# Performance work log

Measured on AMD Instinct MI355X. Metric: run time of the kernel, lower is better.

The kernel has to match this reference:

```python
import jax, jax.numpy as jnp
import numpy as np

EPS = 1e-8


def setup_inputs() -> dict:
    key = jax.random.key(0)
    k1, k2, k3, k4 = jax.random.split(key, 4)
    B, N, M, C = 512, 512, 128, 1024
    addr = M + 6  # read head: k(M) + beta(1) + g(1) + s(3) + gamma(1)
    controller_out = jax.random.normal(k1, (B, C), dtype=jnp.float32)
    prev_w = jax.random.uniform(k2, (B, N), dtype=jnp.float32)
    prev_w = prev_w / prev_w.sum(axis=1, keepdims=True)  # valid weighting
    memory_state = jax.random.normal(k3, (B, N, M), dtype=jnp.float32)
    W_fc = jax.random.normal(k4, (C, addr), dtype=jnp.float32) * 0.02
    b_fc = jnp.zeros((addr,), dtype=jnp.float32)
    return {"controller_out": controller_out, "prev_w": prev_w,
            "memory_state": memory_state, "W_fc": W_fc, "b_fc": b_fc}


def reference(controller_out, prev_w, memory_state, W_fc, b_fc):
    M = memory_state.shape[2]
    out = controller_out @ W_fc + b_fc  # [B, M+6]
    k = out[:, :M]                                   # key
    beta = jax.nn.softplus(out[:, M:M + 1])          # key strength
    g = jax.nn.sigmoid(out[:, M + 1:M + 2])          # interpolation gate
    s = jax.nn.softmax(out[:, M + 2:M + 5], axis=1)  # 3-tap shift weights
    gamma = 1.0 + jax.nn.softplus(out[:, M + 5:M + 6])

    # Content addressing (Eq. 5-6): cosine similarity + sharpened softmax
    norm_k = jnp.linalg.norm(k, axis=1, keepdims=True) + EPS      # [B,1]
    norm_mem = jnp.linalg.norm(memory_state, axis=2) + EPS        # [B,N]
    sim = jnp.einsum('bnm,bm->bn', memory_state, k) / (norm_k * norm_mem)
    w_c = jax.nn.softmax(beta * sim, axis=1)

    # Interpolation (Eq. 7)
    w_g = g * w_c + (1.0 - g) * prev_w

    # Circular 3-tap shift (Eq. 8): vectorized roll instead of per-slot loop
    w_s = (s[:, 0:1] * jnp.roll(w_g, 1, axis=1)
           + s[:, 1:2] * w_g
           + s[:, 2:3] * jnp.roll(w_g, -1, axis=1))

    # Sharpening (Eq. 9)
    w_pow = w_s ** gamma
    w = w_pow / (w_pow.sum(axis=1, keepdims=True) + EPS)

    # Read vector (read head)
    read_vec = jnp.einsum('bn,bnm->bm', w, memory_state)
    return (read_vec, w)
```

## Files before the change

### kernel.cpp

```cpp
#include <hip/hip_runtime.h>
#include <math.h>

#define BB   512
#define NN   512
#define MM   128
#define CC   1024
#define ADDR 134
#define EPSF 1e-8f
#define NT   1024

__device__ __forceinline__ float softplus_f(float x) {
    return fmaxf(x, 0.0f) + log1pf(expf(-fabsf(x)));
}

__global__ __launch_bounds__(NT) void ntm_head_kernel(
    const float* __restrict__ co,
    const float* __restrict__ prev_w,
    const float* __restrict__ mem,
    const float* __restrict__ W_fc,
    const float* __restrict__ b_fc,
    float* __restrict__ out_rv,
    float* __restrict__ out_w)
{
    __shared__ __align__(16) float s_co[CC];
    __shared__ __align__(16) float s_k[MM];
    __shared__ float s_extra[8];
    __shared__ float s_fcpart[4 * ADDR];
    __shared__ float s_bsim[NN];
    __shared__ float s_wg[NN];
    __shared__ float s_w[NN];
    __shared__ __align__(16) float s_part[32 * MM];
    __shared__ float s_red[16];
    __shared__ float s_params[8];

    const int t = threadIdx.x;
    const int b = blockIdx.x;
    const int wv = t >> 6;

    s_co[t] = co[(size_t)b * CC + t];
    __syncthreads();

    {
        const int q = t >> 8;
        const int j = t & 255;
        if (j < ADDR) {
            float a0 = 0.f, a1 = 0.f, a2 = 0.f, a3 = 0.f;
            const float* Wp = W_fc + j;
            const int c0 = q * 256;
            for (int c = c0; c < c0 + 256; c += 4) {
                float4 cv = *(const float4*)(s_co + c);
                a0 = fmaf(cv.x, Wp[(size_t)(c + 0) * ADDR], a0);
                a1 = fmaf(cv.y, Wp[(size_t)(c + 1) * ADDR], a1);
                a2 = fmaf(cv.z, Wp[(size_t)(c + 2) * ADDR], a2);
                a3 = fmaf(cv.w, Wp[(size_t)(c + 3) * ADDR], a3);
            }
            s_fcpart[q * ADDR + j] = (a0 + a1) + (a2 + a3);
        }
    }
    __syncthreads();
    if (t < ADDR) {
        float r = s_fcpart[t] + s_fcpart[ADDR + t] + s_fcpart[2 * ADDR + t]
                + s_fcpart[3 * ADDR + t] + b_fc[t];
        if (t < MM) s_k[t] = r; else s_extra[t - MM] = r;
    }
    __syncthreads();

    {
        float v = (t < MM) ? s_k[t] * s_k[t] : 0.0f;
        #pragma unroll
        for (int off = 32; off >= 1; off >>= 1) v += __shfl_xor(v, off, 64);
        if ((t & 63) == 0) s_red[wv] = v;
        __syncthreads();
        if (t == 0) {
            float ks = 0.f;
            #pragma unroll
            for (int i = 0; i < 16; ++i) ks += s_red[i];
            float norm_k = sqrtf(ks) + EPSF;
            float beta = softplus_f(s_extra[0]);
            float g = 1.0f / (1.0f + expf(-s_extra[1]));
            float e0 = s_extra[2], e1 = s_extra[3], e2 = s_extra[4];
            float mx = fmaxf(e0, fmaxf(e1, e2));
            float x0 = expf(e0 - mx), x1 = expf(e1 - mx), x2 = expf(e2 - mx);
            float inv = 1.0f / (x0 + x1 + x2);
            s_params[0] = beta / norm_k;
            s_params[1] = g;
            s_params[2] = x0 * inv;
            s_params[3] = x1 * inv;
            s_params[4] = x2 * inv;
            s_params[5] = 1.0f + softplus_f(s_extra[5]);
        }
    }
    __syncthreads();

    const float bnk = s_params[0];
    const float4* memb = (const float4*)(mem + (size_t)b * NN * MM);

    {
        const int gi = t >> 5;
        const int l  = t & 31;
        float4 kv = ((const float4*)s_k)[l];
        for (int n0 = gi; n0 < NN; n0 += 128) {
            float4 a0 = memb[(size_t)(n0      ) * 32 + l];
            float4 a1 = memb[(size_t)(n0 + 32 ) * 32 + l];
            float4 a2 = memb[(size_t)(n0 + 64 ) * 32 + l];
            float4 a3 = memb[(size_t)(n0 + 96 ) * 32 + l];
            float d0 = a0.x*kv.x + a0.y*kv.y + a0.z*kv.z + a0.w*kv.w;
            float q0 = a0.x*a0.x + a0.y*a0.y + a0.z*a0.z + a0.w*a0.w;
            float d1 = a1.x*kv.x + a1.y*kv.y + a1.z*kv.z + a1.w*kv.w;
            float q1 = a1.x*a1.x + a1.y*a1.y + a1.z*a1.z + a1.w*a1.w;
            float d2 = a2.x*kv.x + a2.y*kv.y + a2.z*kv.z + a2.w*kv.w;
            float q2 = a2.x*a2.x + a2.y*a2.y + a2.z*a2.z + a2.w*a2.w;
            float d3 = a3.x*kv.x + a3.y*kv.y + a3.z*kv.z + a3.w*kv.w;
            float q3 = a3.x*a3.x + a3.y*a3.y + a3.z*a3.z + a3.w*a3.w;
            #pragma unroll
            for (int off = 16; off >= 1; off >>= 1) {
                d0 += __shfl_xor(d0, off, 64); q0 += __shfl_xor(q0, off, 64);
                d1 += __shfl_xor(d1, off, 64); q1 += __shfl_xor(q1, off, 64);
                d2 += __shfl_xor(d2, off, 64); q2 += __shfl_xor(q2, off, 64);
                d3 += __shfl_xor(d3, off, 64); q3 += __shfl_xor(q3, off, 64);
            }
            if (l == 0) {
                s_bsim[n0      ] = bnk * d0 / (sqrtf(q0) + EPSF);
                s_bsim[n0 + 32 ] = bnk * d1 / (sqrtf(q1) + EPSF);
                s_bsim[n0 + 64 ] = bnk * d2 / (sqrtf(q2) + EPSF);
                s_bsim[n0 + 96 ] = bnk * d3 / (sqrtf(q3) + EPSF);
            }
        }
    }
    __syncthreads();

    {
        const bool act = (t < NN);
        float bv = act ? s_bsim[t] : -INFINITY;
        float pw = act ? prev_w[(size_t)b * NN + t] : 0.0f;

        float m = bv;
        #pragma unroll
        for (int off = 32; off >= 1; off >>= 1) m = fmaxf(m, __shfl_xor(m, off, 64));
        if ((t & 63) == 0) s_red[wv] = m;
        __syncthreads();
        float M8 = -INFINITY;
        #pragma unroll
        for (int i = 0; i < 8; ++i) M8 = fmaxf(M8, s_red[i]);
        __syncthreads();

        float e = act ? expf(bv - M8) : 0.0f;
        float ls = e;
        #pragma unroll
        for (int off = 32; off >= 1; off >>= 1) ls += __shfl_xor(ls, off, 64);
        if ((t & 63) == 0) s_red[wv] = ls;
        __syncthreads();
        float S = 0.f;
        #pragma unroll
        for (int i = 0; i < 16; ++i) S += s_red[i];
        __syncthreads();

        const float invS = 1.0f / S;
        const float g = s_params[1];
        float wg = fmaf(g, e * invS, (1.0f - g) * pw);
        if (act) s_wg[t] = wg;
        __syncthreads();

        const float sh0 = s_params[2], sh1 = s_params[3], sh2 = s_params[4];
        const float gamma = s_params[5];
        float wp = 0.0f;
        if (act) {
            float ws = sh0 * s_wg[(t + NN - 1) & (NN - 1)] + sh1 * wg
                     + sh2 * s_wg[(t + 1) & (NN - 1)];
            wp = powf(ws, gamma);
        }
        float lz = wp;
        #pragma unroll
        for (int off = 32; off >= 1; off >>= 1) lz += __shfl_xor(lz, off, 64);
        if ((t & 63) == 0) s_red[wv] = lz;
        __syncthreads();
        float Z = 0.f;
        #pragma unroll
        for (int i = 0; i < 16; ++i) Z += s_red[i];

        const float invZ = 1.0f / (Z + EPSF);
        if (act) {
            float w = wp * invZ;
            s_w[t] = w;
            out_w[(size_t)b * NN + t] = w;
        }
    }
    __syncthreads();

    {
        const int q = t >> 5;
        const int l = t & 31;
        float4 acc = make_float4(0.f, 0.f, 0.f, 0.f);
        const int nb = q * 16;
        #pragma unroll
        for (int i = 0; i < 16; i += 4) {
            const int n = nb + i;
            float4 a0 = memb[(size_t)(n    ) * 32 + l];
            float4 a1 = memb[(size_t)(n + 1) * 32 + l];
            float4 a2 = memb[(size_t)(n + 2) * 32 + l];
            float4 a3 = memb[(size_t)(n + 3) * 32 + l];
            float w0 = s_w[n], w1 = s_w[n + 1], w2 = s_w[n + 2], w3 = s_w[n + 3];
            acc.x = fmaf(w0, a0.x, acc.x); acc.y = fmaf(w0, a0.y, acc.y);
            acc.z = fmaf(w0, a0.z, acc.z); acc.w = fmaf(w0, a0.w, acc.w);
            acc.x = fmaf(w1, a1.x, acc.x); acc.y = fmaf(w1, a1.y, acc.y);
            acc.z = fmaf(w1, a1.z, acc.z); acc.w = fmaf(w1, a1.w, acc.w);
            acc.x = fmaf(w2, a2.x, acc.x); acc.y = fmaf(w2, a2.y, acc.y);
            acc.z = fmaf(w2, a2.z, acc.z); acc.w = fmaf(w2, a2.w, acc.w);
            acc.x = fmaf(w3, a3.x, acc.x); acc.y = fmaf(w3, a3.y, acc.y);
            acc.z = fmaf(w3, a3.z, acc.z); acc.w = fmaf(w3, a3.w, acc.w);
        }
        *((float4*)&s_part[q * MM + l * 4]) = acc;
        __syncthreads();
        if (t < MM) {
            float r = 0.f;
            #pragma unroll
            for (int q2 = 0; q2 < 32; ++q2) r += s_part[q2 * MM + t];
            out_rv[(size_t)b * MM + t] = r;
        }
    }
}

extern "C" void kernel_launch(void* const* d_in, const int* in_sizes, int n_in,
                              void* d_out, int out_size, void* d_ws, size_t ws_size,
                              hipStream_t stream) {
    const float* co     = (const float*)d_in[0];
    const float* prev_w = (const float*)d_in[1];
    const float* mem    = (const float*)d_in[2];
    const float* W_fc   = (const float*)d_in[3];
    const float* b_fc   = (const float*)d_in[4];
    float* out = (float*)d_out;
    ntm_head_kernel<<<BB, NT, 0, stream>>>(co, prev_w, mem, W_fc, b_fc,
                                           out, out + (size_t)BB * MM);
}
```

Baseline: 245.9 us.

## Split FC projection into separate kernel and restructure similarity pass with 4-lane rows

Moves the controller FC projection and head-parameter computation into a separate kernel that handles two batch rows per block and writes key and parameters to a workspace. The main kernel then reads those from the workspace instead of recomputing the FC, which frees the 1024-thread blocks from the serial FC phase. The similarity pass changes to four lanes per memory row with the row-max reduction fused in, removing a sync and one reduction pass. This adds a second launch and a workspace round trip, and the FC kernel has low parallelism with only 192 threads per block.

```diff
diff --git a/kernel.cpp b/kernel.cpp
--- a/kernel.cpp
+++ b/kernel.cpp
@@ -7,88 +7,111 @@
 #define CC   1024
 #define ADDR 134
 #define EPSF 1e-8f
-#define NT   1024
+#define WSSTRIDE 136
 
 __device__ __forceinline__ float softplus_f(float x) {
     return fmaxf(x, 0.0f) + log1pf(expf(-fabsf(x)));
 }
 
-__global__ __launch_bounds__(NT) void ntm_head_kernel(
+__global__ __launch_bounds__(192) void ntm_fc_kernel(
     const float* __restrict__ co,
+    const float* __restrict__ W_fc,
+    const float* __restrict__ b_fc,
+    float* __restrict__ ws)
+{
+    __shared__ __align__(16) float s_co[2 * CC];
+    __shared__ float s_nr[2][2];
+    __shared__ float s_ex[2][8];
+
+    const int t = threadIdx.x;
+    const int b0 = blockIdx.x * 2;
+
+    {
+        const float4* src = (const float4*)(co + (size_t)b0 * CC);
+        float4* dst = (float4*)s_co;
+        for (int i = t; i < 512; i += 192) dst[i] = src[i];
+    }
+    __syncthreads();
+
+    float k0 = 0.f, k1 = 0.f;
+    if (t < ADDR) {
+        float a00 = 0.f, a01 = 0.f, a10 = 0.f, a11 = 0.f;
+        const float* Wj = W_fc + t;
+        for (int c = 0; c < CC; c += 8) {
+            float wv[8];
+            #pragma unroll
+            for (int i = 0; i < 8; ++i) wv[i] = Wj[(size_t)(c + i) * ADDR];
+            #pragma unroll
+            for (int i = 0; i < 8; ++i) {
+                if (i & 1) { a01 = fmaf(wv[i], s_co[c + i], a01);
+                             a11 = fmaf(wv[i], s_co[CC + c + i], a11); }
+                else       { a00 = fmaf(wv[i], s_co[c + i], a00);
+                             a10 = fmaf(wv[i], s_co[CC + c + i], a10); }
+            }
+        }
+        float bias = b_fc[t];
+        k0 = a00 + a01 + bias;
+        k1 = a10 + a11 + bias;
+        if (t >= MM) { s_ex[0][t - MM] = k0; s_ex[1][t - MM] = k1; }
+        else {
+            ws[(size_t)b0 * WSSTRIDE + t] = k0;
+            ws[(size_t)(b0 + 1) * WSSTRIDE + t] = k1;
+        }
+    }
+    if (t < MM) {
+        float v0 = k0 * k0, v1 = k1 * k1;
+        #pragma unroll
+        for (int off = 32; off >= 1; off >>= 1) {
+            v0 += __shfl_xor(v0, off, 64);
+            v1 += __shfl_xor(v1, off, 64);
+        }
+        if ((t & 63) == 0) { s_nr[t >> 6][0] = v0; s_nr[t >> 6][1] = v1; }
+    }
+    __syncthreads();
+    if (t < 2) {
+        float ks = s_nr[0][t] + s_nr[1][t];
+        float norm_k = sqrtf(ks) + EPSF;
+        float beta = softplus_f(s_ex[t][0]);
+        float g = 1.0f / (1.0f + expf(-s_ex[t][1]));
+        float e0 = s_ex[t][2], e1 = s_ex[t][3], e2 = s_ex[t][4];
+        float mx = fmaxf(e0, fmaxf(e1, e2));
+        float x0 = expf(e0 - mx), x1 = expf(e1 - mx), x2 = expf(e2 - mx);
+        float inv = 1.0f / (x0 + x1 + x2);
+        float* p = ws + (size_t)(b0 + t) * WSSTRIDE + MM;
+        p[0] = beta / norm_k;
+        p[1] = g;
+        p[2] = x0 * inv;
+        p[3] = x1 * inv;
+        p[4] = x2 * inv;
+        p[5] = 1.0f + softplus_f(s_ex[t][5]);
+    }
+}
+
+__global__ __launch_bounds__(1024) void ntm_main_kernel(
     const float* __restrict__ prev_w,
     const float* __restrict__ mem,
-    const float* __restrict__ W_fc,
-    const float* __restrict__ b_fc,
+    const float* __restrict__ ws,
     float* __restrict__ out_rv,
     float* __restrict__ out_w)
 {
-    __shared__ __align__(16) float s_co[CC];
     __shared__ __align__(16) float s_k[MM];
-    __shared__ float s_extra[8];
-    __shared__ float s_fcpart[4 * ADDR];
+    __shared__ float s_params[8];
     __shared__ float s_bsim[NN];
     __shared__ float s_wg[NN];
     __shared__ float s_w[NN];
     __shared__ __align__(16) float s_part[32 * MM];
-    __shared__ float s_red[16];
-    __shared__ float s_params[8];
+    __shared__ float s_redA[16];
+    __shared__ float s_redB[16];
 
     const int t = threadIdx.x;
     const int b = blockIdx.x;
     const int wv = t >> 6;
 
-    s_co[t] = co[(size_t)b * CC + t];
-    __syncthreads();
-
-    {
-        const int q = t >> 8;
-        const int j = t & 255;
-        if (j < ADDR) {
-            float a0 = 0.f, a1 = 0.f, a2 = 0.f, a3 = 0.f;
-            const float* Wp = W_fc + j;
-            const int c0 = q * 256;
-            for (int c = c0; c < c0 + 256; c += 4) {
-                float4 cv = *(const float4*)(s_co + c);
-                a0 = fmaf(cv.x, Wp[(size_t)(c + 0) * ADDR], a0);
-                a1 = fmaf(cv.y, Wp[(size_t)(c + 1) * ADDR], a1);
-                a2 = fmaf(cv.z, Wp[(size_t)(c + 2) * ADDR], a2);
-                a3 = fmaf(cv.w, Wp[(size_t)(c + 3) * ADDR], a3);
-            }
-            s_fcpart[q * ADDR + j] = (a0 + a1) + (a2 + a3);
-        }
-    }
-    __syncthreads();
-    if (t < ADDR) {
-        float r = s_fcpart[t] + s_fcpart[ADDR + t] + s_fcpart[2 * ADDR + t]
-                + s_fcpart[3 * ADDR + t] + b_fc[t];
-        if (t < MM) s_k[t] = r; else s_extra[t - MM] = r;
-    }
-    __syncthreads();
-
-    {
-        float v = (t < MM) ? s_k[t] * s_k[t] : 0.0f;
-        #pragma unroll
-        for (int off = 32; off >= 1; off >>= 1) v += __shfl_xor(v, off, 64);
-        if ((t & 63) == 0) s_red[wv] = v;
-        __syncthreads();
-        if (t == 0) {
-            float ks = 0.f;
-            #pragma unroll
-            for (int i = 0; i < 16; ++i) ks += s_red[i];
-            float norm_k = sqrtf(ks) + EPSF;
-            float beta = softplus_f(s_extra[0]);
-            float g = 1.0f / (1.0f + expf(-s_extra[1]));
-            float e0 = s_extra[2], e1 = s_extra[3], e2 = s_extra[4];
-            float mx = fmaxf(e0, fmaxf(e1, e2));
-            float x0 = expf(e0 - mx), x1 = expf(e1 - mx), x2 = expf(e2 - mx);
-            float inv = 1.0f / (x0 + x1 + x2);
-            s_params[0] = beta / norm_k;
-            s_params[1] = g;
-            s_params[2] = x0 * inv;
-            s_params[3] = x1 * inv;
-            s_params[4] = x2 * inv;
-            s_params[5] = 1.0f + softplus_f(s_extra[5]);
-        }
+    float pw = (t < NN) ? prev_w[(size_t)b * NN + t] : 0.0f;
+
+    if (t < WSSTRIDE) {
+        float v = ws[(size_t)b * WSSTRIDE + t];
+        if (t < MM) s_k[t] = v; else s_params[t - MM] = v;
     }
     __syncthreads();
 
@@ -96,91 +119,80 @@
     const float4* memb = (const float4*)(mem + (size_t)b * NN * MM);
 
     {
-        const int gi = t >> 5;
-        const int l  = t & 31;
-        float4 kv = ((const float4*)s_k)[l];
-        for (int n0 = gi; n0 < NN; n0 += 128) {
-            float4 a0 = memb[(size_t)(n0      ) * 32 + l];
-            float4 a1 = memb[(size_t)(n0 + 32 ) * 32 + l];
-            float4 a2 = memb[(size_t)(n0 + 64 ) * 32 + l];
-            float4 a3 = memb[(size_t)(n0 + 96 ) * 32 + l];
-            float d0 = a0.x*kv.x + a0.y*kv.y + a0.z*kv.z + a0.w*kv.w;
-            float q0 = a0.x*a0.x + a0.y*a0.y + a0.z*a0.z + a0.w*a0.w;
-            float d1 = a1.x*kv.x + a1.y*kv.y + a1.z*kv.z + a1.w*kv.w;
-            float q1 = a1.x*a1.x + a1.y*a1.y + a1.z*a1.z + a1.w*a1.w;
-            float d2 = a2.x*kv.x + a2.y*kv.y + a2.z*kv.z + a2.w*kv.w;
-            float q2 = a2.x*a2.x + a2.y*a2.y + a2.z*a2.z + a2.w*a2.w;
-            float d3 = a3.x*kv.x + a3.y*kv.y + a3.z*kv.z + a3.w*kv.w;
-            float q3 = a3.x*a3.x + a3.y*a3.y + a3.z*a3.z + a3.w*a3.w;
-            #pragma unroll
-            for (int off = 16; off >= 1; off >>= 1) {
-                d0 += __shfl_xor(d0, off, 64); q0 += __shfl_xor(q0, off, 64);
-                d1 += __shfl_xor(d1, off, 64); q1 += __shfl_xor(q1, off, 64);
-                d2 += __shfl_xor(d2, off, 64); q2 += __shfl_xor(q2, off, 64);
-                d3 += __shfl_xor(d3, off, 64); q3 += __shfl_xor(q3, off, 64);
+        const int l4 = t & 3;
+        const int row0 = t >> 2;
+        float4 kf[8];
+        #pragma unroll
+        for (int i = 0; i < 8; ++i) kf[i] = ((const float4*)s_k)[l4 + 4 * i];
+
+        float maxv = -INFINITY;
+        #pragma unroll
+        for (int it = 0; it < 2; ++it) {
+            const int row = row0 + it * 256;
+            const float4* rp = memb + (size_t)row * 32;
+            float4 a[8];
+            #pragma unroll
+            for (int i = 0; i < 8; ++i) a[i] = rp[l4 + 4 * i];
+            float d = 0.f, q = 0.f;
+            #pragma unroll
+            for (int i = 0; i < 8; ++i) {
+                d = fmaf(a[i].x, kf[i].x, d); q = fmaf(a[i].x, a[i].x, q);
+                d = fmaf(a[i].y, kf[i].y, d); q = fmaf(a[i].y, a[i].y, q);
+                d = fmaf(a[i].z, kf[i].z, d); q = fmaf(a[i].z, a[i].z, q);
+                d = fmaf(a[i].w, kf[i].w, d); q = fmaf(a[i].w, a[i].w, q);
             }
-            if (l == 0) {
-                s_bsim[n0      ] = bnk * d0 / (sqrtf(q0) + EPSF);
-                s_bsim[n0 + 32 ] = bnk * d1 / (sqrtf(q1) + EPSF);
-                s_bsim[n0 + 64 ] = bnk * d2 / (sqrtf(q2) + EPSF);
-                s_bsim[n0 + 96 ] = bnk * d3 / (sqrtf(q3) + EPSF);
-            }
-        }
-    }
-    __syncthreads();
+            d += __shfl_xor(d, 1, 64); q += __shfl_xor(q, 1, 64);
+            d += __shfl_xor(d, 2, 64); q += __shfl_xor(q, 2, 64);
+            float bsim = bnk * d / (sqrtf(q) + EPSF);
+            maxv = fmaxf(maxv, bsim);
+            if (l4 == 0) s_bsim[row] = bsim;
+        }
+        #pragma unroll
+        for (int off = 32; off >= 1; off >>= 1) maxv = fmaxf(maxv, __shfl_xor(maxv, off, 64));
+        if ((t & 63) == 0) s_redA[wv] = maxv;
+    }
+    __syncthreads();
+
+    float Mx = -INFINITY;
+    #pragma unroll
+    for (int i = 0; i < 16; ++i) Mx = fmaxf(Mx, s_redA[i]);
 
     {
         const bool act = (t < NN);
-        float bv = act ? s_bsim[t] : -INFINITY;
-        float pw = act ? prev_w[(size_t)b * NN + t] : 0.0f;
-
-        float m = bv;
-        #pragma unroll
-        for (int off = 32; off >= 1; off >>= 1) m = fmaxf(m, __shfl_xor(m, off, 64));
-        if ((t & 63) == 0) s_red[wv] = m;
-        __syncthreads();
-        float M8 = -INFINITY;
-        #pragma unroll
-        for (int i = 0; i < 8; ++i) M8 = fmaxf(M8, s_red[i]);
-        __syncthreads();
-
-        float e = act ? expf(bv - M8) : 0.0f;
+        float e = act ? expf(s_bsim[t] - Mx) : 0.0f;
         float ls = e;
         #pragma unroll
         for (int off = 32; off >= 1; off >>= 1) ls += __shfl_xor(ls, off, 64);
-        if ((t & 63) == 0) s_red[wv] = ls;
+        if ((t & 63) == 0) s_redB[wv] = ls;
         __syncthreads();
         float S = 0.f;
         #pragma unroll
-        for (int i = 0; i < 16; ++i) S += s_red[i];
-        __syncthreads();
+        for (int i = 0; i < 16; ++i) S += s_redB[i];
 
         const float invS = 1.0f / S;
         const float g = s_params[1];
-        float wg = fmaf(g, e * invS, (1.0f - g) * pw);
-        if (act) s_wg[t] = wg;
-        __syncthreads();
-
-        const float sh0 = s_params[2], sh1 = s_params[3], sh2 = s_params[4];
-        const float gamma = s_params[5];
+        float wg = 0.0f;
+        if (act) { wg = fmaf(g, e * invS, (1.0f - g) * pw); s_wg[t] = wg; }
+        __syncthreads();
+
         float wp = 0.0f;
         if (act) {
-            float ws = sh0 * s_wg[(t + NN - 1) & (NN - 1)] + sh1 * wg
-                     + sh2 * s_wg[(t + 1) & (NN - 1)];
-            wp = powf(ws, gamma);
+            float wsv = s_params[2] * s_wg[(t + NN - 1) & (NN - 1)]
+                      + s_params[3] * wg
+                      + s_params[4] * s_wg[(t + 1) & (NN - 1)];
+            wp = powf(wsv, s_params[5]);
         }
         float lz = wp;
         #pragma unroll
         for (int off = 32; off >= 1; off >>= 1) lz += __shfl_xor(lz, off, 64);
-        if ((t & 63) == 0) s_red[wv] = lz;
+        if ((t & 63) == 0) s_redA[wv] = lz;
         __syncthreads();
         float Z = 0.f;
         #pragma unroll
-        for (int i = 0; i < 16; ++i) Z += s_red[i];
-
-        const float invZ = 1.0f / (Z + EPSF);
+        for (int i = 0; i < 16; ++i) Z += s_redA[i];
+
         if (act) {
-            float w = wp * invZ;
+            float w = wp / (Z + EPSF);
             s_w[t] = w;
             out_w[(size_t)b * NN + t] = w;
         }
@@ -229,6 +241,9 @@
     const float* W_fc   = (const float*)d_in[3];
     const float* b_fc   = (const float*)d_in[4];
     float* out = (float*)d_out;
-    ntm_head_kernel<<<BB, NT, 0, stream>>>(co, prev_w, mem, W_fc, b_fc,
-                                           out, out + (size_t)BB * MM);
-}
+    float* ws  = (float*)d_ws;
+
+    ntm_fc_kernel<<<BB / 2, 192, 0, stream>>>(co, W_fc, b_fc, ws);
+    ntm_main_kernel<<<BB, 1024, 0, stream>>>(prev_w, mem, ws,
+                                             out, out + (size_t)BB * MM);
+}
```

New measurement: 258.0 us. 4.9% more time.

## Hold the memory tile in registers to read it once and drop the softmax max pass

Applied to the files above, without the earlier changes.

Each thread now loads its four memory rows into registers at kernel start, before the FC projection. The same registers serve both the cosine-similarity pass and the read-vector pass, so memory_state is read from global memory once instead of twice, and the load overlaps the FC work. The block shrinks to 512 threads with launch bounds (512, 2). The separate max reduction in the content softmax is removed, and the read-vector partials are combined with shuffles plus a small shared buffer. The trade-offs are very high register pressure, with 128 floats of tile per thread and a risk of spills, and exponentials that are not max-subtracted, which could overflow for large beta.

```diff
diff --git a/kernel.cpp b/kernel.cpp
--- a/kernel.cpp
+++ b/kernel.cpp
@@ -7,13 +7,12 @@
 #define CC   1024
 #define ADDR 134
 #define EPSF 1e-8f
-#define NT   1024
 
 __device__ __forceinline__ float softplus_f(float x) {
     return fmaxf(x, 0.0f) + log1pf(expf(-fabsf(x)));
 }
 
-__global__ __launch_bounds__(NT) void ntm_head_kernel(
+__global__ __launch_bounds__(512, 2) void ntm_fused_kernel(
     const float* __restrict__ co,
     const float* __restrict__ prev_w,
     const float* __restrict__ mem,
@@ -23,152 +22,130 @@
     float* __restrict__ out_w)
 {
     __shared__ __align__(16) float s_co[CC];
+    __shared__ float s_fcp[2][ADDR];
     __shared__ __align__(16) float s_k[MM];
-    __shared__ float s_extra[8];
-    __shared__ float s_fcpart[4 * ADDR];
-    __shared__ float s_bsim[NN];
+    __shared__ float s_ex[8];
+    __shared__ float s_params[8];
+    __shared__ float s_e[NN];
     __shared__ float s_wg[NN];
     __shared__ float s_w[NN];
-    __shared__ __align__(16) float s_part[32 * MM];
-    __shared__ float s_red[16];
-    __shared__ float s_params[8];
-
-    const int t = threadIdx.x;
-    const int b = blockIdx.x;
-    const int wv = t >> 6;
-
-    s_co[t] = co[(size_t)b * CC + t];
-    __syncthreads();
-
-    {
-        const int q = t >> 8;
-        const int j = t & 255;
-        if (j < ADDR) {
-            float a0 = 0.f, a1 = 0.f, a2 = 0.f, a3 = 0.f;
-            const float* Wp = W_fc + j;
-            const int c0 = q * 256;
-            for (int c = c0; c < c0 + 256; c += 4) {
-                float4 cv = *(const float4*)(s_co + c);
-                a0 = fmaf(cv.x, Wp[(size_t)(c + 0) * ADDR], a0);
-                a1 = fmaf(cv.y, Wp[(size_t)(c + 1) * ADDR], a1);
-                a2 = fmaf(cv.z, Wp[(size_t)(c + 2) * ADDR], a2);
-                a3 = fmaf(cv.w, Wp[(size_t)(c + 3) * ADDR], a3);
-            }
-            s_fcpart[q * ADDR + j] = (a0 + a1) + (a2 + a3);
-        }
+    __shared__ float s_red[8];
+    __shared__ __align__(16) float4 s_comb[8][4][8];
+
+    const int t    = threadIdx.x;
+    const int b    = blockIdx.x;
+    const int wv   = t >> 6;
+    const int l4   = t & 3;
+    const int row0 = t >> 2;
+
+    const float4* memb = (const float4*)(mem + (size_t)b * NN * MM);
+    float4 a[4][8];
+    #pragma unroll
+    for (int it = 0; it < 4; ++it) {
+        const float4* rp = memb + (size_t)(row0 + 128 * it) * 32;
+        #pragma unroll
+        for (int i = 0; i < 8; ++i) a[it][i] = rp[l4 + 4 * i];
+    }
+    float pw = prev_w[(size_t)b * NN + t];
+
+    if (t < 256) ((float4*)s_co)[t] = ((const float4*)(co + (size_t)b * CC))[t];
+    __syncthreads();
+
+    if (t < 2 * ADDR) {
+        const int grp = (t >= ADDR) ? 1 : 0;
+        const int j   = t - grp * ADDR;
+        const int c0  = grp << 9;
+        const float* Wj = W_fc + j;
+        float a0 = 0.f, a1 = 0.f, a2 = 0.f, a3 = 0.f;
+        for (int c = 0; c < 512; c += 8) {
+            const int cc = c0 + c;
+            a0 = fmaf(Wj[(size_t)(cc + 0) * ADDR], s_co[cc + 0], a0);
+            a1 = fmaf(Wj[(size_t)(cc + 1) * ADDR], s_co[cc + 1], a1);
+            a2 = fmaf(Wj[(size_t)(cc + 2) * ADDR], s_co[cc + 2], a2);
+            a3 = fmaf(Wj[(size_t)(cc + 3) * ADDR], s_co[cc + 3], a3);
+            a0 = fmaf(Wj[(size_t)(cc + 4) * ADDR], s_co[cc + 4], a0);
+            a1 = fmaf(Wj[(size_t)(cc + 5) * ADDR], s_co[cc + 5], a1);
+            a2 = fmaf(Wj[(size_t)(cc + 6) * ADDR], s_co[cc + 6], a2);
+            a3 = fmaf(Wj[(size_t)(cc + 7) * ADDR], s_co[cc + 7], a3);
+        }
+        s_fcp[grp][j] = (a0 + a1) + (a2 + a3);
     }
     __syncthreads();
     if (t < ADDR) {
-        float r = s_fcpart[t] + s_fcpart[ADDR + t] + s_fcpart[2 * ADDR + t]
-                + s_fcpart[3 * ADDR + t] + b_fc[t];
-        if (t < MM) s_k[t] = r; else s_extra[t - MM] = r;
-    }
-    __syncthreads();
-
-    {
-        float v = (t < MM) ? s_k[t] * s_k[t] : 0.0f;
+        float r = s_fcp[0][t] + s_fcp[1][t] + b_fc[t];
+        if (t < MM) s_k[t] = r; else s_ex[t - MM] = r;
+    }
+    __syncthreads();
+
+    {
+        float v = (t < MM) ? s_k[t] * s_k[t] : 0.f;
         #pragma unroll
         for (int off = 32; off >= 1; off >>= 1) v += __shfl_xor(v, off, 64);
         if ((t & 63) == 0) s_red[wv] = v;
+    }
+    __syncthreads();
+    if (t == 0) {
+        float ks = 0.f;
+        #pragma unroll
+        for (int i = 0; i < 8; ++i) ks += s_red[i];
+        float norm_k = sqrtf(ks) + EPSF;
+        float beta = softplus_f(s_ex[0]);
+        float g = 1.0f / (1.0f + expf(-s_ex[1]));
+        float e0 = s_ex[2], e1 = s_ex[3], e2 = s_ex[4];
+        float mx = fmaxf(e0, fmaxf(e1, e2));
+        float x0 = expf(e0 - mx), x1 = expf(e1 - mx), x2 = expf(e2 - mx);
+        float inv = 1.0f / (x0 + x1 + x2);
+        s_params[0] = beta / norm_k;
+        s_params[1] = g;
+        s_params[2] = x0 * inv;
+        s_params[3] = x1 * inv;
+        s_params[4] = x2 * inv;
+        s_params[5] = 1.0f + softplus_f(s_ex[5]);
+    }
+    __syncthreads();
+
+    {
+        const float bnk = s_params[0];
+        float4 kf[8];
+        #pragma unroll
+        for (int i = 0; i < 8; ++i) kf[i] = ((const float4*)s_k)[l4 + 4 * i];
+        float el = 0.f;
+        #pragma unroll
+        for (int it = 0; it < 4; ++it) {
+            float d = 0.f, q = 0.f;
+            #pragma unroll
+            for (int i = 0; i < 8; ++i) {
+                float4 av = a[it][i];
+                d = fmaf(av.x, kf[i].x, d); q = fmaf(av.x, av.x, q);
+                d = fmaf(av.y, kf[i].y, d); q = fmaf(av.y, av.y, q);
+                d = fmaf(av.z, kf[i].z, d); q = fmaf(av.z, av.z, q);
+                d = fmaf(av.w, kf[i].w, d); q = fmaf(av.w, av.w, q);
+            }
+            d += __shfl_xor(d, 1, 64); q += __shfl_xor(q, 1, 64);
+            d += __shfl_xor(d, 2, 64); q += __shfl_xor(q, 2, 64);
+            float e = expf(bnk * d / (sqrtf(q) + EPSF));
+            if (l4 == 0) { s_e[row0 + 128 * it] = e; el += e; }
+        }
+        #pragma unroll
+        for (int off = 32; off >= 1; off >>= 1) el += __shfl_xor(el, off, 64);
+        if ((t & 63) == 0) s_red[wv] = el;
+    }
+    __syncthreads();
+
+    {
+        float S = 0.f;
+        #pragma unroll
+        for (int i = 0; i < 8; ++i) S += s_red[i];
+        const float g = s_params[1];
+        float wg = fmaf(g, s_e[t] / S, (1.0f - g) * pw);
+        s_wg[t] = wg;
         __syncthreads();
-        if (t == 0) {
-            float ks = 0.f;
-            #pragma unroll
-            for (int i = 0; i < 16; ++i) ks += s_red[i];
-            float norm_k = sqrtf(ks) + EPSF;
-            float beta = softplus_f(s_extra[0]);
-            float g = 1.0f / (1.0f + expf(-s_extra[1]));
-            float e0 = s_extra[2], e1 = s_extra[3], e2 = s_extra[4];
-            float mx = fmaxf(e0, fmaxf(e1, e2));
-            float x0 = expf(e0 - mx), x1 = expf(e1 - mx), x2 = expf(e2 - mx);
-            float inv = 1.0f / (x0 + x1 + x2);
-            s_params[0] = beta / norm_k;
-            s_params[1] = g;
-            s_params[2] = x0 * inv;
-            s_params[3] = x1 * inv;
-            s_params[4] = x2 * inv;
-            s_params[5] = 1.0f + softplus_f(s_extra[5]);
-        }
-    }
-    __syncthreads();
-
-    const float bnk = s_params[0];
-    const float4* memb = (const float4*)(mem + (size_t)b * NN * MM);
-
-    {
-        const int gi = t >> 5;
-        const int l  = t & 31;
-        float4 kv = ((const float4*)s_k)[l];
-        for (int n0 = gi; n0 < NN; n0 += 128) {
-            float4 a0 = memb[(size_t)(n0      ) * 32 + l];
-            float4 a1 = memb[(size_t)(n0 + 32 ) * 32 + l];
-            float4 a2 = memb[(size_t)(n0 + 64 ) * 32 + l];
-            float4 a3 = memb[(size_t)(n0 + 96 ) * 32 + l];
-            float d0 = a0.x*kv.x + a0.y*kv.y + a0.z*kv.z + a0.w*kv.w;
-            float q0 = a0.x*a0.x + a0.y*a0.y + a0.z*a0.z + a0.w*a0.w;
-            float d1 = a1.x*kv.x + a1.y*kv.y + a1.z*kv.z + a1.w*kv.w;
-            float q1 = a1.x*a1.x + a1.y*a1.y + a1.z*a1.z + a1.w*a1.w;
-            float d2 = a2.x*kv.x + a2.y*kv.y + a2.z*kv.z + a2.w*kv.w;
-            float q2 = a2.x*a2.x + a2.y*a2.y + a2.z*a2.z + a2.w*a2.w;
-            float d3 = a3.x*kv.x + a3.y*kv.y + a3.z*kv.z + a3.w*kv.w;
-            float q3 = a3.x*a3.x + a3.y*a3.y + a3.z*a3.z + a3.w*a3.w;
-            #pragma unroll
-            for (int off = 16; off >= 1; off >>= 1) {
-                d0 += __shfl_xor(d0, off, 64); q0 += __shfl_xor(q0, off, 64);
-                d1 += __shfl_xor(d1, off, 64); q1 += __shfl_xor(q1, off, 64);
-                d2 += __shfl_xor(d2, off, 64); q2 += __shfl_xor(q2, off, 64);
-                d3 += __shfl_xor(d3, off, 64); q3 += __shfl_xor(q3, off, 64);
-            }
-            if (l == 0) {
-                s_bsim[n0      ] = bnk * d0 / (sqrtf(q0) + EPSF);
-                s_bsim[n0 + 32 ] = bnk * d1 / (sqrtf(q1) + EPSF);
-                s_bsim[n0 + 64 ] = bnk * d2 / (sqrtf(q2) + EPSF);
-                s_bsim[n0 + 96 ] = bnk * d3 / (sqrtf(q3) + EPSF);
-            }
-        }
-    }
-    __syncthreads();
-
-    {
-        const bool act = (t < NN);
-        float bv = act ? s_bsim[t] : -INFINITY;
-        float pw = act ? prev_w[(size_t)b * NN + t] : 0.0f;
-
-        float m = bv;
-        #pragma unroll
-        for (int off = 32; off >= 1; off >>= 1) m = fmaxf(m, __shfl_xor(m, off, 64));
-        if ((t & 63) == 0) s_red[wv] = m;
-        __syncthreads();
-        float M8 = -INFINITY;
-        #pragma unroll
-        for (int i = 0; i < 8; ++i) M8 = fmaxf(M8, s_red[i]);
-        __syncthreads();
-
-        float e = act ? expf(bv - M8) : 0.0f;
-        float ls = e;
-        #pragma unroll
-        for (int off = 32; off >= 1; off >>= 1) ls += __shfl_xor(ls, off, 64);
-        if ((t & 63) == 0) s_red[wv] = ls;
-        __syncthreads();
-        float S = 0.f;
-        #pragma unroll
-        for (int i = 0; i < 16; ++i) S += s_red[i];
-        __syncthreads();
-
-        const float invS = 1.0f / S;
-        const float g = s_params[1];
-        float wg = fmaf(g, e * invS, (1.0f - g) * pw);
-        if (act) s_wg[t] = wg;
-        __syncthreads();
-
-        const float sh0 = s_params[2], sh1 = s_params[3], sh2 = s_params[4];
-        const float gamma = s_params[5];
-        float wp = 0.0f;
-        if (act) {
-            float ws = sh0 * s_wg[(t + NN - 1) & (NN - 1)] + sh1 * wg
-                     + sh2 * s_wg[(t + 1) & (NN - 1)];
-            wp = powf(ws, gamma);
-        }
+
+        float wsv = s_params[2] * s_wg[(t + NN - 1) & (NN - 1)]
+                  + s_params[3] * wg
+                  + s_params[4] * s_wg[(t + 1) & (NN - 1)];
+        float wp = powf(wsv, s_params[5]);
+
         float lz = wp;
         #pragma unroll
         for (int off = 32; off >= 1; off >>= 1) lz += __shfl_xor(lz, off, 64);
@@ -176,45 +153,51 @@
         __syncthreads();
         float Z = 0.f;
         #pragma unroll
-        for (int i = 0; i < 16; ++i) Z += s_red[i];
-
-        const float invZ = 1.0f / (Z + EPSF);
-        if (act) {
-            float w = wp * invZ;
-            s_w[t] = w;
-            out_w[(size_t)b * NN + t] = w;
-        }
-    }
-    __syncthreads();
-
-    {
-        const int q = t >> 5;
-        const int l = t & 31;
-        float4 acc = make_float4(0.f, 0.f, 0.f, 0.f);
-        const int nb = q * 16;
-        #pragma unroll
-        for (int i = 0; i < 16; i += 4) {
-            const int n = nb + i;
-            float4 a0 = memb[(size_t)(n    ) * 32 + l];
-            float4 a1 = memb[(size_t)(n + 1) * 32 + l];
-            float4 a2 = memb[(size_t)(n + 2) * 32 + l];
-            float4 a3 = memb[(size_t)(n + 3) * 32 + l];
-            float w0 = s_w[n], w1 = s_w[n + 1], w2 = s_w[n + 2], w3 = s_w[n + 3];
-            acc.x = fmaf(w0, a0.x, acc.x); acc.y = fmaf(w0, a0.y, acc.y);
-            acc.z = fmaf(w0, a0.z, acc.z); acc.w = fmaf(w0, a0.w, acc.w);
-            acc.x = fmaf(w1, a1.x, acc.x); acc.y = fmaf(w1, a1.y, acc.y);
-            acc.z = fmaf(w1, a1.z, acc.z); acc.w = fmaf(w1, a1.w, acc.w);
-            acc.x = fmaf(w2, a2.x, acc.x); acc.y = fmaf(w2, a2.y, acc.y);
-            acc.z = fmaf(w2, a2.z, acc.z); acc.w = fmaf(w2, a2.w, acc.w);
-            acc.x = fmaf(w3, a3.x, acc.x); acc.y = fmaf(w3, a3.y, acc.y);
-            acc.z = fmaf(w3, a3.z, acc.z); acc.w = fmaf(w3, a3.w, acc.w);
-        }
-        *((float4*)&s_part[q * MM + l * 4]) = acc;
+        for (int i = 0; i < 8; ++i) Z += s_red[i];
+
+        float w = wp / (Z + EPSF);
+        s_w[t] = w;
+        out_w[(size_t)b * NN + t] = w;
+    }
+    __syncthreads();
+
+    {
+        float4 acc[8];
+        #pragma unroll
+        for (int i = 0; i < 8; ++i) acc[i] = make_float4(0.f, 0.f, 0.f, 0.f);
+        #pragma unroll
+        for (int it = 0; it < 4; ++it) {
+            float wr = s_w[row0 + 128 * it];
+            #pragma unroll
+            for (int i = 0; i < 8; ++i) {
+                float4 av = a[it][i];
+                acc[i].x = fmaf(wr, av.x, acc[i].x);
+                acc[i].y = fmaf(wr, av.y, acc[i].y);
+                acc[i].z = fmaf(wr, av.z, acc[i].z);
+                acc[i].w = fmaf(wr, av.w, acc[i].w);
+            }
+        }
+        #pragma unroll
+        for (int mask = 4; mask <= 32; mask <<= 1) {
+            #pragma unroll
+            for (int i = 0; i < 8; ++i) {
+                acc[i].x += __shfl_xor(acc[i].x, mask, 64);
+                acc[i].y += __shfl_xor(acc[i].y, mask, 64);
+                acc[i].z += __shfl_xor(acc[i].z, mask, 64);
+                acc[i].w += __shfl_xor(acc[i].w, mask, 64);
+            }
+        }
+        if (((t >> 2) & 15) == 0) {
+            #pragma unroll
+            for (int i = 0; i < 8; ++i) s_comb[wv][l4][i] = acc[i];
+        }
         __syncthreads();
         if (t < MM) {
+            const int F = t >> 2, cl4 = F & 3, ii = F >> 2, comp = t & 3;
             float r = 0.f;
             #pragma unroll
-            for (int q2 = 0; q2 < 32; ++q2) r += s_part[q2 * MM + t];
+            for (int w8 = 0; w8 < 8; ++w8)
+                r += ((const float*)&s_comb[w8][cl4][ii])[comp];
             out_rv[(size_t)b * MM + t] = r;
         }
     }
@@ -229,6 +212,6 @@
     const float* W_fc   = (const float*)d_in[3];
     const float* b_fc   = (const float*)d_in[4];
     float* out = (float*)d_out;
-    ntm_head_kernel<<<BB, NT, 0, stream>>>(co, prev_w, mem, W_fc, b_fc,
-                                           out, out + (size_t)BB * MM);
+    ntm_fused_kernel<<<BB, 512, 0, stream>>>(co, prev_w, mem, W_fc, b_fc,
+                                             out, out + (size_t)BB * MM);
 }
```

Result: no change. 242.1 us (-1.5%).
